# Kernel optimization log

Measured on AMD Instinct MI355X. Metric: run time of the kernel, lower is better.

## Reference

```python
import jax, jax.numpy as jnp
from jax import lax
import numpy as np

IN_F, H1, OUT_F, P = 128, 64, 64, 0.25
B, T = 64, 2048


def setup_inputs() -> dict:
    key = jax.random.key(0)
    ks = jax.random.split(key, 12)
    def w(k, shape, fan_in):
        return jax.random.normal(k, shape, dtype=jnp.float32) / np.sqrt(fan_in).astype(np.float32)
    x = jax.random.normal(ks[0], (B, T, IN_F), dtype=jnp.float32)
    # PyTorch LSTM param layout: W_ih [4H, in], W_hh [4H, H], gate order i,f,g,o
    W_ih1 = w(ks[1], (4 * H1, IN_F), IN_F)
    W_hh1 = w(ks[2], (4 * H1, H1), H1)
    b_ih1 = jnp.zeros((4 * H1,), jnp.float32)
    b_hh1 = jnp.zeros((4 * H1,), jnp.float32)
    W_ih2 = w(ks[3], (4 * OUT_F, H1), H1)
    W_hh2 = w(ks[4], (4 * OUT_F, OUT_F), OUT_F)
    b_ih2 = jnp.zeros((4 * OUT_F,), jnp.float32)
    b_hh2 = jnp.zeros((4 * OUT_F,), jnp.float32)
    # Variational (locked) dropout masks: one per sequence, shared across timesteps,
    # inverted-dropout pre-scaled by 1/(1-p).
    keep = 1.0 - P
    mask1 = (jax.random.bernoulli(ks[5], keep, (B, H1)).astype(jnp.float32) / keep)
    mask2 = (jax.random.bernoulli(ks[6], keep, (B, OUT_F)).astype(jnp.float32) / keep)
    return {"x": x, "W_ih1": W_ih1, "W_hh1": W_hh1, "b_ih1": b_ih1, "b_hh1": b_hh1,
            "W_ih2": W_ih2, "W_hh2": W_hh2, "b_ih2": b_ih2, "b_hh2": b_hh2,
            "mask1": mask1, "mask2": mask2}


def _lstm(x, W_ih, W_hh, b_ih, b_hh):
    # x: [B,T,I]; returns all hidden states [B,T,H]
    Bd = x.shape[0]
    H = W_hh.shape[1]
    # Precompute input contribution for all timesteps (one big GEMM).
    xg = jnp.einsum('bti,gi->btg', x, W_ih) + b_ih + b_hh  # [B,T,4H]
    W_hh_T = W_hh.T  # [H,4H]
    def step(carry, xg_t):
        h, c = carry
        g = xg_t + h @ W_hh_T
        i, f, gg, o = jnp.split(g, 4, axis=-1)
        c = jax.nn.sigmoid(f) * c + jax.nn.sigmoid(i) * jnp.tanh(gg)
        h = jax.nn.sigmoid(o) * jnp.tanh(c)
        return (h, c), h
    h0 = jnp.zeros((Bd, H), x.dtype)
    c0 = jnp.zeros((Bd, H), x.dtype)
    _, hs = lax.scan(step, (h0, c0), jnp.swapaxes(xg, 0, 1))
    return jnp.swapaxes(hs, 0, 1)


def reference(x, W_ih1, W_hh1, b_ih1, b_hh1, W_ih2, W_hh2, b_ih2, b_hh2, mask1, mask2):
    out = _lstm(x, W_ih1, W_hh1, b_ih1, b_hh1) * mask1[:, None, :]
    out = _lstm(out, W_ih2, W_hh2, b_ih2, b_hh2) * mask2[:, None, :]
    return jax.nn.relu(out)
```

## Files before the change

kernel.cpp:

```cpp
#include <hip/hip_runtime.h>
#include <hip/hip_bf16.h>

#define BB 64
#define TT 2048
#define INF 128
#define HH 64
#define GG 256

__device__ __forceinline__ float sigm(float x) { return 1.0f / (1.0f + __expf(-x)); }
__device__ __forceinline__ float tanh_f(float x) {
  float e = __expf(2.0f * x);
  return 1.0f - 2.0f / (e + 1.0f);
}
__device__ __forceinline__ float bcast(float v, int l) {
  return __uint_as_float(__builtin_amdgcn_readlane(__float_as_uint(v), l));
}
__device__ __forceinline__ void lstm_upd(float Si, float Sf, float Tg, float So,
                                         float& c, float& h) {
  c = fmaf(Sf, c, Si * Tg);
  h = So * tanh_f(c);
}


#define WL2(I)                                                                   \
  { float4 a_ = p[lane * 16 + (I)];                                              \
    wA[4*(I)] = a_.x; wA[4*(I)+1] = a_.y; wA[4*(I)+2] = a_.z; wA[4*(I)+3] = a_.w;\
    float4 b_ = p[(64 + lane) * 16 + (I)];                                       \
    wB[4*(I)] = b_.x; wB[4*(I)+1] = b_.y; wB[4*(I)+2] = b_.z; wB[4*(I)+3] = b_.w; }
#define WL2x4(I) WL2(I) WL2((I)+1) WL2((I)+2) WL2((I)+3)
#define WLOAD2 WL2x4(0) WL2x4(4) WL2x4(8) WL2x4(12)

#define G1(K)                                                    \
  { float hk = bcast(hv, (K));                                   \
    aA = fmaf(hk, wA[(K)], aA); aB = fmaf(hk, wB[(K)], aB); }
#define G8(K) G1(K) G1((K)+1) G1((K)+2) G1((K)+3) G1((K)+4) G1((K)+5) G1((K)+6) G1((K)+7)
#define DOT2G G8(0) G8(8) G8(16) G8(24) G8(32) G8(40) G8(48) G8(56)

#define YW1(I) { float4 a_ = Wp[t * 32 + (I)];                                   \
    wr[4*(I)] = a_.x; wr[4*(I)+1] = a_.y; wr[4*(I)+2] = a_.z; wr[4*(I)+3] = a_.w; }
#define YW4(I) YW1(I) YW1((I)+1) YW1((I)+2) YW1((I)+3)
#define YWLOAD YW4(0) YW4(4) YW4(8) YW4(12) YW4(16) YW4(20) YW4(24) YW4(28)

#define YD1(L)                                                   \
  { float xa = bcast(curx, (L)); float xb = bcast(cury, (L));    \
    ae = fmaf(xa, wr[2*(L)], ae); ao = fmaf(xb, wr[2*(L)+1], ao); }
#define YD8(L) YD1(L) YD1((L)+1) YD1((L)+2) YD1((L)+3) YD1((L)+4) YD1((L)+5) YD1((L)+6) YD1((L)+7)
#define YDOT64 YD8(0) YD8(8) YD8(16) YD8(24) YD8(32) YD8(40) YD8(48) YD8(56)

__global__ __launch_bounds__(256, 1) void xgemm(const float* __restrict__ X,
                                                const float* __restrict__ W,
                                                const float* __restrict__ bi,
                                                const float* __restrict__ bh,
                                                float* __restrict__ XG) {
  const int t = threadIdx.x;
  const int lane = t & 63;
  const long m0 = (long)blockIdx.x * 256;

  float wr[INF];
  const float4* Wp = (const float4*)W;
  YWLOAD
  const float bias = bi[t] + bh[t];

  const float2* Xp = (const float2*)X;
  float2 cur = Xp[(size_t)m0 * 64 + lane];
  float2 nx1 = Xp[(size_t)(m0 + 1) * 64 + lane];

  for (int mi = 0; mi < 256; ++mi) {
    const long m = m0 + mi;
    float2 nx2 = make_float2(0.f, 0.f);
    if (mi + 2 < 256) nx2 = Xp[(size_t)(m + 2) * 64 + lane];

    const float curx = cur.x, cury = cur.y;
    float ae = bias, ao = 0.f;
    YDOT64
    XG[(size_t)m * GG + t] = ae + ao;
    cur = nx1; nx1 = nx2;
  }
}

__global__ __launch_bounds__(384, 1) void lstm2(const float* __restrict__ XG,
                                                const float* __restrict__ Whh1,
                                                const float* __restrict__ Wih2,
                                                const float* __restrict__ Whh2,
                                                const float* __restrict__ bi2,
                                                const float* __restrict__ bh2,
                                                const float* __restrict__ m1g,
                                                const float* __restrict__ m2g,
                                                float* __restrict__ out) {
  const int b = blockIdx.x;
  const int wid = threadIdx.x >> 6;
  const int lane = threadIdx.x & 63;

  __shared__ int f_0A, f_0B, f_h1, f_xA, f_xB, f_2A, f_2B;
  __shared__ __align__(16) float ex0A[2][2 * HH];
  __shared__ __align__(16) float ex0B[2][2 * HH];
  __shared__ __align__(16) float ex2A[2][2 * HH];
  __shared__ __align__(16) float ex2B[2][2 * HH];
  __shared__ __align__(16) float x2buf[8][HH];
  __shared__ __align__(16) float a2xA[8][2 * HH];
  __shared__ __align__(16) float a2xB[8][2 * HH];

  if (threadIdx.x == 0) { f_0A = 0; f_0B = 0; f_h1 = 0; f_xA = 0; f_xB = 0; f_2A = 0; f_2B = 0; }
  __syncthreads();

#define WAITC(seen, flag, tgt)                                  \
  do {                                                          \
    if ((seen) < (tgt)) {                                       \
      while (((seen) = *(volatile int*)&(flag)) < (tgt)) {}     \
    }                                                           \
    asm volatile("" ::: "memory");                              \
  } while (0)
#define PUBLISH(flag, val)                                      \
  do {                                                          \
    asm volatile("s_waitcnt lgkmcnt(0)" ::: "memory");          \
    if (lane == 0) *(volatile int*)&(flag) = (val);             \
  } while (0)

  if (wid == 2) {
    float wA[HH], wB[HH];
    const float4* p = (const float4*)Whh1;
    WLOAD2
    const float m1 = m1g[b * HH + lane];
    const float* xgp = XG + (size_t)b * TT * GG;

    float xi0 = xgp[lane],      xf0 = xgp[64 + lane];
    float xi1 = xgp[GG + lane], xf1 = xgp[GG + 64 + lane];

    float h1 = 0.f, c1 = 0.f;
    int s0B = 0, sxa = 0, sxb = 0;
    for (int s = 0; s < TT; ++s) {
      float xi2 = 0.f, xf2 = 0.f;
      if (s + 2 < TT) {
        const float* q = xgp + (size_t)(s + 2) * GG;
        xi2 = q[lane]; xf2 = q[64 + lane];
      }
      const float hv = h1;
      float aA = xi0, aB = xf0;
      DOT2G
      const float Si = sigm(aA), Sf = sigm(aB);
      ex0A[s & 1][lane] = Si; ex0A[s & 1][64 + lane] = Sf;
      PUBLISH(f_0A, s + 1);
      WAITC(s0B, f_0B, s + 1);
      const float Tg = ex0B[s & 1][lane], So = ex0B[s & 1][64 + lane];
      lstm_upd(Si, Sf, Tg, So, c1, h1);
      WAITC(sxa, f_xA, s - 7);
      WAITC(sxb, f_xB, s - 7);
      x2buf[s & 7][lane] = h1 * m1;
      PUBLISH(f_h1, s + 1);
      xi0 = xi1; xf0 = xf1; xi1 = xi2; xf1 = xf2;
    }
  } else if (wid == 0) {
    float wA[HH], wB[HH];
    const float4* p = (const float4*)(Whh1 + 128 * HH);
    WLOAD2
    const float* xgp = XG + (size_t)b * TT * GG;

    float xg0 = xgp[128 + lane],      xo0 = xgp[192 + lane];
    float xg1 = xgp[GG + 128 + lane], xo1 = xgp[GG + 192 + lane];

    float h1 = 0.f, c1 = 0.f;
    int s0A = 0;
    for (int s = 0; s < TT; ++s) {
      float xg2 = 0.f, xo2 = 0.f;
      if (s + 2 < TT) {
        const float* q = xgp + (size_t)(s + 2) * GG;
        xg2 = q[128 + lane]; xo2 = q[192 + lane];
      }
      const float hv = h1;
      float aA = xg0, aB = xo0;
      DOT2G
      const float Tg = tanh_f(aA), So = sigm(aB);
      ex0B[s & 1][lane] = Tg; ex0B[s & 1][64 + lane] = So;
      PUBLISH(f_0B, s + 1);
      WAITC(s0A, f_0A, s + 1);
      const float Si = ex0A[s & 1][lane], Sf = ex0A[s & 1][64 + lane];
      lstm_upd(Si, Sf, Tg, So, c1, h1);
      xg0 = xg1; xo0 = xo1; xg1 = xg2; xo1 = xo2;
    }
  } else if (wid == 4) {
    float wA[HH], wB[HH];
    const float4* p = (const float4*)Wih2;
    WLOAD2
    const float biA = bi2[lane] + bh2[lane];
    const float biB = bi2[64 + lane] + bh2[64 + lane];

    int sh = 0, sc = 0;
    for (int s = 0; s < TT; ++s) {
      WAITC(sh, f_h1, s + 1);
      const float hv = x2buf[s & 7][lane];
      float aA = biA, aB = biB;
      DOT2G
      WAITC(sc, f_2A, s - 7);
      a2xA[s & 7][lane] = aA; a2xA[s & 7][64 + lane] = aB;
      PUBLISH(f_xA, s + 1);
    }
  } else if (wid == 5) {
    float wA[HH], wB[HH];
    const float4* p = (const float4*)(Wih2 + 128 * HH);
    WLOAD2
    const float biA = bi2[128 + lane] + bh2[128 + lane];
    const float biB = bi2[192 + lane] + bh2[192 + lane];

    int sh = 0, sc = 0;
    for (int s = 0; s < TT; ++s) {
      WAITC(sh, f_h1, s + 1);
      const float hv = x2buf[s & 7][lane];
      float aA = biA, aB = biB;
      DOT2G
      WAITC(sc, f_2B, s - 7);
      a2xB[s & 7][lane] = aA; a2xB[s & 7][64 + lane] = aB;
      PUBLISH(f_xB, s + 1);
    }
  } else if (wid == 3) {
    float wA[HH], wB[HH];
    const float4* p = (const float4*)Whh2;
    WLOAD2
    const float m2v = m2g[b * HH + lane];
    float* ob = out + (size_t)b * TT * HH;

    float h2 = 0.f, c2 = 0.f;
    int sx = 0, s2B = 0;
    for (int s = 0; s < TT; ++s) {
      WAITC(sx, f_xA, s + 1);
      const float pi = a2xA[s & 7][lane], pf = a2xA[s & 7][64 + lane];
      const float hv = h2;
      float aA = 0.f, aB = 0.f;
      DOT2G
      aA += pi; aB += pf;
      const float Si = sigm(aA), Sf = sigm(aB);
      ex2A[s & 1][lane] = Si; ex2A[s & 1][64 + lane] = Sf;
      PUBLISH(f_2A, s + 1);
      WAITC(s2B, f_2B, s + 1);
      const float Tg = ex2B[s & 1][lane], So = ex2B[s & 1][64 + lane];
      lstm_upd(Si, Sf, Tg, So, c2, h2);
      ob[(size_t)s * HH + lane] = fmaxf(h2 * m2v, 0.f);
    }
  } else {
    float wA[HH], wB[HH];
    const float4* p = (const float4*)(Whh2 + 128 * HH);
    WLOAD2

    float h2 = 0.f, c2 = 0.f;
    int sx = 0, s2A = 0;
    for (int s = 0; s < TT; ++s) {
      WAITC(sx, f_xB, s + 1);
      const float pg = a2xB[s & 7][lane], po = a2xB[s & 7][64 + lane];
      const float hv = h2;
      float aA = 0.f, aB = 0.f;
      DOT2G
      aA += pg; aB += po;
      const float Tg = tanh_f(aA), So = sigm(aB);
      ex2B[s & 1][lane] = Tg; ex2B[s & 1][64 + lane] = So;
      PUBLISH(f_2B, s + 1);
      WAITC(s2A, f_2A, s + 1);
      const float Si = ex2A[s & 1][lane], Sf = ex2A[s & 1][64 + lane];
      lstm_upd(Si, Sf, Tg, So, c2, h2);
    }
  }
#undef WAITC
#undef PUBLISH
}

extern "C" void kernel_launch(void* const* d_in, const int* in_sizes, int n_in,
                              void* d_out, int out_size, void* d_ws, size_t ws_size,
                              hipStream_t stream) {
  (void)in_sizes; (void)n_in; (void)out_size; (void)ws_size;
  const float* x     = (const float*)d_in[0];
  const float* W_ih1 = (const float*)d_in[1];
  const float* W_hh1 = (const float*)d_in[2];
  const float* b_ih1 = (const float*)d_in[3];
  const float* b_hh1 = (const float*)d_in[4];
  const float* W_ih2 = (const float*)d_in[5];
  const float* W_hh2 = (const float*)d_in[6];
  const float* b_ih2 = (const float*)d_in[7];
  const float* b_hh2 = (const float*)d_in[8];
  const float* mask1 = (const float*)d_in[9];
  const float* mask2 = (const float*)d_in[10];
  float* out = (float*)d_out;

  float* xg1 = (float*)d_ws;

  xgemm<<<dim3(BB * TT / 256), dim3(256), 0, stream>>>(x, W_ih1, b_ih1, b_hh1, xg1);
  lstm2<<<dim3(BB), dim3(384), 0, stream>>>(xg1, W_hh1, W_ih2, W_hh2, b_ih2, b_hh2,
                                            mask1, mask2, out);
}
```

Measured before the change: 2.729 ms.

## Split layer-2 input projection warps by even/odd timestep parity

Raises the block from six to eight waves. The two warps that computed the layer-2 input projection become four, split by even and odd timesteps, each with its own progress flag. The aim is to keep the input-projection stage off the critical path, so each projection warp has two steps of slack per element. In exchange there is extra register and weight-load cost, more flags to poll, and more waves contending for the SIMDs.

```diff
diff --git a/kernel.cpp b/kernel.cpp
--- a/kernel.cpp
+++ b/kernel.cpp
@@ -78,29 +78,36 @@
   }
 }
 
-__global__ __launch_bounds__(384, 1) void lstm2(const float* __restrict__ XG,
-                                                const float* __restrict__ Whh1,
-                                                const float* __restrict__ Wih2,
-                                                const float* __restrict__ Whh2,
-                                                const float* __restrict__ bi2,
-                                                const float* __restrict__ bh2,
-                                                const float* __restrict__ m1g,
-                                                const float* __restrict__ m2g,
-                                                float* __restrict__ out) {
+__global__ __launch_bounds__(512, 1)
+void lstm2(const float* __restrict__ XG,
+           const float* __restrict__ Whh1,
+           const float* __restrict__ Wih2,
+           const float* __restrict__ Whh2,
+           const float* __restrict__ bi2,
+           const float* __restrict__ bh2,
+           const float* __restrict__ m1g,
+           const float* __restrict__ m2g,
+           float* __restrict__ out) {
   const int b = blockIdx.x;
   const int wid = threadIdx.x >> 6;
   const int lane = threadIdx.x & 63;
 
-  __shared__ int f_0A, f_0B, f_h1, f_xA, f_xB, f_2A, f_2B;
+  __shared__ int f_0A, f_0B;
+  __shared__ int f_2A, f_2B;
+  __shared__ int f_h1;
+  __shared__ int f_xife, f_xifo, f_xgoe, f_xgoo;
   __shared__ __align__(16) float ex0A[2][2 * HH];
   __shared__ __align__(16) float ex0B[2][2 * HH];
   __shared__ __align__(16) float ex2A[2][2 * HH];
   __shared__ __align__(16) float ex2B[2][2 * HH];
   __shared__ __align__(16) float x2buf[8][HH];
-  __shared__ __align__(16) float a2xA[8][2 * HH];
-  __shared__ __align__(16) float a2xB[8][2 * HH];
-
-  if (threadIdx.x == 0) { f_0A = 0; f_0B = 0; f_h1 = 0; f_xA = 0; f_xB = 0; f_2A = 0; f_2B = 0; }
+  __shared__ __align__(16) float a2xif[8][2 * HH];
+  __shared__ __align__(16) float a2xgo[8][2 * HH];
+
+  if (threadIdx.x == 0) {
+    f_0A = 0; f_0B = 0; f_2A = 0; f_2B = 0; f_h1 = 0;
+    f_xife = 0; f_xifo = 0; f_xgoe = 0; f_xgoo = 0;
+  }
   __syncthreads();
 
 #define WAITC(seen, flag, tgt)                                  \
@@ -116,7 +123,7 @@
     if (lane == 0) *(volatile int*)&(flag) = (val);             \
   } while (0)
 
-  if (wid == 2) {
+  if (wid == 0) {
     float wA[HH], wB[HH];
     const float4* p = (const float4*)Whh1;
     WLOAD2
@@ -127,7 +134,7 @@
     float xi1 = xgp[GG + lane], xf1 = xgp[GG + 64 + lane];
 
     float h1 = 0.f, c1 = 0.f;
-    int s0B = 0, sxa = 0, sxb = 0;
+    int s0B = 0, se1 = 0, se2 = 0, so1 = 0, so2 = 0;
     for (int s = 0; s < TT; ++s) {
       float xi2 = 0.f, xf2 = 0.f;
       if (s + 2 < TT) {
@@ -143,13 +150,13 @@
       WAITC(s0B, f_0B, s + 1);
       const float Tg = ex0B[s & 1][lane], So = ex0B[s & 1][64 + lane];
       lstm_upd(Si, Sf, Tg, So, c1, h1);
-      WAITC(sxa, f_xA, s - 7);
-      WAITC(sxb, f_xB, s - 7);
+      if (s & 1) { WAITC(so1, f_xifo, s - 7); WAITC(so2, f_xgoo, s - 7); }
+      else       { WAITC(se1, f_xife, s - 7); WAITC(se2, f_xgoe, s - 7); }
       x2buf[s & 7][lane] = h1 * m1;
       PUBLISH(f_h1, s + 1);
       xi0 = xi1; xf0 = xf1; xi1 = xi2; xf1 = xf2;
     }
-  } else if (wid == 0) {
+  } else if (wid == 1) {
     float wA[HH], wB[HH];
     const float4* p = (const float4*)(Whh1 + 128 * HH);
     WLOAD2
@@ -177,41 +184,7 @@
       lstm_upd(Si, Sf, Tg, So, c1, h1);
       xg0 = xg1; xo0 = xo1; xg1 = xg2; xo1 = xo2;
     }
-  } else if (wid == 4) {
-    float wA[HH], wB[HH];
-    const float4* p = (const float4*)Wih2;
-    WLOAD2
-    const float biA = bi2[lane] + bh2[lane];
-    const float biB = bi2[64 + lane] + bh2[64 + lane];
-
-    int sh = 0, sc = 0;
-    for (int s = 0; s < TT; ++s) {
-      WAITC(sh, f_h1, s + 1);
-      const float hv = x2buf[s & 7][lane];
-      float aA = biA, aB = biB;
-      DOT2G
-      WAITC(sc, f_2A, s - 7);
-      a2xA[s & 7][lane] = aA; a2xA[s & 7][64 + lane] = aB;
-      PUBLISH(f_xA, s + 1);
-    }
-  } else if (wid == 5) {
-    float wA[HH], wB[HH];
-    const float4* p = (const float4*)(Wih2 + 128 * HH);
-    WLOAD2
-    const float biA = bi2[128 + lane] + bh2[128 + lane];
-    const float biB = bi2[192 + lane] + bh2[192 + lane];
-
-    int sh = 0, sc = 0;
-    for (int s = 0; s < TT; ++s) {
-      WAITC(sh, f_h1, s + 1);
-      const float hv = x2buf[s & 7][lane];
-      float aA = biA, aB = biB;
-      DOT2G
-      WAITC(sc, f_2B, s - 7);
-      a2xB[s & 7][lane] = aA; a2xB[s & 7][64 + lane] = aB;
-      PUBLISH(f_xB, s + 1);
-    }
-  } else if (wid == 3) {
+  } else if (wid == 2) {
     float wA[HH], wB[HH];
     const float4* p = (const float4*)Whh2;
     WLOAD2
@@ -219,10 +192,12 @@
     float* ob = out + (size_t)b * TT * HH;
 
     float h2 = 0.f, c2 = 0.f;
-    int sx = 0, s2B = 0;
+    int sxe = 0, sxo = 0, s2B = 0;
     for (int s = 0; s < TT; ++s) {
-      WAITC(sx, f_xA, s + 1);
-      const float pi = a2xA[s & 7][lane], pf = a2xA[s & 7][64 + lane];
+      if (s & 1) { WAITC(sxo, f_xifo, s + 1); }
+      else       { WAITC(sxe, f_xife, s + 1); }
+      const float pi = a2xif[s & 7][lane];
+      const float pf = a2xif[s & 7][64 + lane];
       const float hv = h2;
       float aA = 0.f, aB = 0.f;
       DOT2G
@@ -235,16 +210,18 @@
       lstm_upd(Si, Sf, Tg, So, c2, h2);
       ob[(size_t)s * HH + lane] = fmaxf(h2 * m2v, 0.f);
     }
-  } else {
+  } else if (wid == 3) {
     float wA[HH], wB[HH];
     const float4* p = (const float4*)(Whh2 + 128 * HH);
     WLOAD2
 
     float h2 = 0.f, c2 = 0.f;
-    int sx = 0, s2A = 0;
+    int sxe = 0, sxo = 0, s2A = 0;
     for (int s = 0; s < TT; ++s) {
-      WAITC(sx, f_xB, s + 1);
-      const float pg = a2xB[s & 7][lane], po = a2xB[s & 7][64 + lane];
+      if (s & 1) { WAITC(sxo, f_xgoo, s + 1); }
+      else       { WAITC(sxe, f_xgoe, s + 1); }
+      const float pg = a2xgo[s & 7][lane];
+      const float po = a2xgo[s & 7][64 + lane];
       const float hv = h2;
       float aA = 0.f, aB = 0.f;
       DOT2G
@@ -255,6 +232,74 @@
       WAITC(s2A, f_2A, s + 1);
       const float Si = ex2A[s & 1][lane], Sf = ex2A[s & 1][64 + lane];
       lstm_upd(Si, Sf, Tg, So, c2, h2);
+    }
+  } else if (wid == 4) {
+    float wA[HH], wB[HH];
+    const float4* p = (const float4*)Wih2;
+    WLOAD2
+    const float biA = bi2[lane] + bh2[lane];
+    const float biB = bi2[64 + lane] + bh2[64 + lane];
+
+    int s0 = 0, sc = 0;
+    for (int s = 0; s < TT; s += 2) {
+      WAITC(s0, f_h1, s + 1);
+      const float hv = x2buf[s & 7][lane];
+      float aA = biA, aB = biB;
+      DOT2G
+      WAITC(sc, f_2A, s - 7);
+      a2xif[s & 7][lane] = aA; a2xif[s & 7][64 + lane] = aB;
+      PUBLISH(f_xife, s + 1);
+    }
+  } else if (wid == 5) {
+    float wA[HH], wB[HH];
+    const float4* p = (const float4*)Wih2;
+    WLOAD2
+    const float biA = bi2[lane] + bh2[lane];
+    const float biB = bi2[64 + lane] + bh2[64 + lane];
+
+    int s0 = 0, sc = 0;
+    for (int s = 1; s < TT; s += 2) {
+      WAITC(s0, f_h1, s + 1);
+      const float hv = x2buf[s & 7][lane];
+      float aA = biA, aB = biB;
+      DOT2G
+      WAITC(sc, f_2A, s - 7);
+      a2xif[s & 7][lane] = aA; a2xif[s & 7][64 + lane] = aB;
+      PUBLISH(f_xifo, s + 1);
+    }
+  } else if (wid == 6) {
+    float wA[HH], wB[HH];
+    const float4* p = (const float4*)(Wih2 + 128 * HH);
+    WLOAD2
+    const float biA = bi2[128 + lane] + bh2[128 + lane];
+    const float biB = bi2[192 + lane] + bh2[192 + lane];
+
+    int s0 = 0, sc = 0;
+    for (int s = 0; s < TT; s += 2) {
+      WAITC(s0, f_h1, s + 1);
+      const float hv = x2buf[s & 7][lane];
+      float aA = biA, aB = biB;
+      DOT2G
+      WAITC(sc, f_2B, s - 7);
+      a2xgo[s & 7][lane] = aA; a2xgo[s & 7][64 + lane] = aB;
+      PUBLISH(f_xgoe, s + 1);
+    }
+  } else {
+    float wA[HH], wB[HH];
+    const float4* p = (const float4*)(Wih2 + 128 * HH);
+    WLOAD2
+    const float biA = bi2[128 + lane] + bh2[128 + lane];
+    const float biB = bi2[192 + lane] + bh2[192 + lane];
+
+    int s0 = 0, sc = 0;
+    for (int s = 1; s < TT; s += 2) {
+      WAITC(s0, f_h1, s + 1);
+      const float hv = x2buf[s & 7][lane];
+      float aA = biA, aB = biB;
+      DOT2G
+      WAITC(sc, f_2B, s - 7);
+      a2xgo[s & 7][lane] = aA; a2xgo[s & 7][64 + lane] = aB;
+      PUBLISH(f_xgoo, s + 1);
     }
   }
 #undef WAITC
@@ -281,6 +326,6 @@
   float* xg1 = (float*)d_ws;
 
   xgemm<<<dim3(BB * TT / 256), dim3(256), 0, stream>>>(x, W_ih1, b_ih1, b_hh1, xg1);
-  lstm2<<<dim3(BB), dim3(384), 0, stream>>>(xg1, W_hh1, W_ih2, W_hh2, b_ih2, b_hh2,
-                                            mask1, mask2, out);
-}
+  lstm2<<<dim3(BB), dim3(512), 0, stream>>>(xg1, W_hh1, W_ih2, W_hh2,
+                                            b_ih2, b_hh2, mask1, mask2, out);
+}
```

Measured after the change: 2.903 ms. 1.06x slower.
